# Kernel tuning notes

Measured on AMD Instinct MI355X. Metric: run time of the kernel, lower is better.

The kernel has to match this reference:

```python
import jax, jax.numpy as jnp
import numpy as np

B, S, H, E = 64, 1024, 256, 256

def setup_inputs() -> dict:
    key = jax.random.key(0)
    k = jax.random.split(key, 6)
    scale = 1.0 / np.sqrt(H)
    return {
        "data_alpha": jax.random.normal(k[0], (B, S, H), jnp.float32),
        "data_beta": jax.random.normal(k[1], (B, S, H), jnp.float32),
        "data_embed": jax.random.normal(k[2], (B, S, E), jnp.float32),
        "data_mask": jnp.ones((B, S), jnp.float32),
        "Wb": jax.random.normal(k[3], (E, H), jnp.float32) * scale,
        "bb": jnp.zeros((E,), jnp.float32),
        "Wa": jax.random.normal(k[4], (H,), jnp.float32) * scale,
        "ba": jnp.zeros((1,), jnp.float32),
    }

def reference(data_alpha, data_beta, data_embed, data_mask, Wb, bb, Wa, ba):
    # beta gates: tanh(Linear(H->E))  [B,S,E]
    beta_w = jnp.tanh(jnp.einsum('bsh,eh->bse', data_beta, Wb) + bb)
    # alpha logits: Linear(H->1)  [B,S]
    corr = jnp.einsum('bsh,h->bs', data_alpha, Wa) + ba
    attn = jnp.exp(corr)[:, None, :]                       # [B,1,S]
    seq = data_alpha.shape[1]
    flag = jnp.triu(jnp.ones((seq, seq), data_alpha.dtype))[None]  # j >= i
    ef = flag * data_mask[:, None, :]                      # [B,S,S]
    num = attn * ef                                        # [B,S,S]
    acc = jnp.sum(num, axis=-1, keepdims=True) + 1e-10     # [B,S,1]
    alpha = num / acc                                      # [B,S,S]
    ew = beta_w * data_embed                               # [B,S,E]
    return jnp.einsum('bij,bje->bie', alpha, ew)           # [B,S,E]
```

## Files before the change

kernel.cpp:

```cpp
#include <hip/hip_runtime.h>
#include <hip/hip_bf16.h>

#define B_ 64
#define S_ 1024
#define H_ 256
#define E_ 256

#define EG_ 32
#define LDSB_ST 264
#define CH_ 128
#define NCH_ 8

typedef __attribute__((ext_vector_type(8))) __bf16 bf16x8;
typedef __attribute__((ext_vector_type(4))) __bf16 bf16x4;
typedef __attribute__((ext_vector_type(4))) float f32x4;

__global__ __launch_bounds__(256) void k0_prep(
        const float* __restrict__ alpha, const float* __restrict__ mask,
        const float* __restrict__ Wa,    const float* __restrict__ ba,
        const float* __restrict__ Wb,    __bf16* __restrict__ WbBf,
        float* __restrict__ w) {
    const int tid = threadIdx.x, blk = blockIdx.x;
    if (blk < 64) {
        int i = blk * 256 + tid;
        float4 v = ((const float4*)Wb)[i];
        bf16x4 bv;
        bv[0] = (__bf16)v.x; bv[1] = (__bf16)v.y;
        bv[2] = (__bf16)v.z; bv[3] = (__bf16)v.w;
        ((bf16x4*)WbBf)[i] = bv;
    }
    const int pr = tid >> 2, pc = tid & 3;
    const int m = blk * 64 + pr;
    const float4* ar = (const float4*)(alpha + (size_t)m * H_ + pc * 64);
    const float4* wr = (const float4*)(Wa + pc * 64);
    float p = 0.f;
    #pragma unroll
    for (int i = 0; i < 16; ++i) {
        float4 a = ar[i], v = wr[i];
        p += a.x * v.x + a.y * v.y + a.z * v.z + a.w * v.w;
    }
    p += __shfl_xor(p, 1, 64);
    p += __shfl_xor(p, 2, 64);
    if (pc == 0) w[m] = __expf(p + ba[0]) * mask[m];
}

__global__ __launch_bounds__(512, 4) void k2_main(
        const float* __restrict__ beta, const float* __restrict__ embed,
        const __bf16* __restrict__ WbBf, const float* __restrict__ bb,
        const float* __restrict__ w, float* __restrict__ t) {
    __shared__ __bf16 ldsB[EG_ * LDSB_ST];
    __shared__ float wsLds[S_];
    __shared__ float ivLds[S_];
    __shared__ float red[8 * EG_];
    __shared__ float run[EG_];
    __shared__ float wsum[4];

    const int tid = threadIdx.x;
    const int wv = tid >> 6, lane = tid & 63;
    const int l15 = lane & 15, q = lane >> 4;
    const int blk = blockIdx.x;
    const int b  = (blk & 7) * 8 + (blk >> 6);
    const int eg = (blk >> 3) & 7;

    if (tid < 256)
        *(float4*)(wsLds + tid * 4) = *(const float4*)(w + b * S_ + tid * 4);
    {
        const int e = tid >> 4, ks = (tid & 15) * 16;
        const __bf16* src = WbBf + (size_t)(eg * EG_ + e) * H_ + ks;
        *(bf16x8*)(ldsB + e * LDSB_ST + ks)     = *(const bf16x8*)(src);
        *(bf16x8*)(ldsB + e * LDSB_ST + ks + 8) = *(const bf16x8*)(src + 8);
    }
    if (tid < EG_) run[tid] = 0.f;
    __syncthreads();

    {
        float w0 = 0, w1 = 0, w2 = 0, w3 = 0, tot = 0, suf = 0;
        const int sl = tid & 63, sw = tid >> 6;
        if (tid < 256) {
            w0 = wsLds[tid * 4];     w1 = wsLds[tid * 4 + 1];
            w2 = wsLds[tid * 4 + 2]; w3 = wsLds[tid * 4 + 3];
            tot = w0 + w1 + w2 + w3;
            suf = tot;
            #pragma unroll
            for (int off = 1; off < 64; off <<= 1) {
                float o = __shfl_down(suf, off, 64);
                if (sl + off < 64) suf += o;
            }
            if (sl == 0) wsum[sw] = suf;
        }
        __syncthreads();
        if (tid < 256) {
            float waveOff = 0.f;
            for (int j = sw + 1; j < 4; ++j) waveOff += wsum[j];
            float after = (suf - tot) + waveOff;
            float s3 = w3 + after, s2 = w2 + s3, s1 = w1 + s2, s0 = w0 + s1;
            ivLds[tid * 4]     = 1.f / (s0 + 1e-10f);
            ivLds[tid * 4 + 1] = 1.f / (s1 + 1e-10f);
            ivLds[tid * 4 + 2] = 1.f / (s2 + 1e-10f);
            ivLds[tid * 4 + 3] = 1.f / (s3 + 1e-10f);
        }
        __syncthreads();
    }

    const float bb0 = bb[eg * EG_ + l15];
    const float bb1 = bb[eg * EG_ + 16 + l15];

    for (int c = NCH_ - 1; c >= 0; --c) {
        const int rbase = c * CH_ + wv * 16;
        const float* Ar = beta + (size_t)(b * S_ + rbase + l15) * H_ + q * 8;

        f32x4 acc0 = {0.f, 0.f, 0.f, 0.f}, acc1 = {0.f, 0.f, 0.f, 0.f};
        #pragma unroll
        for (int kc = 0; kc < 8; ++kc) {
            float4 a0 = *(const float4*)(Ar + kc * 32);
            float4 a1 = *(const float4*)(Ar + kc * 32 + 4);
            bf16x8 af;
            af[0] = (__bf16)a0.x; af[1] = (__bf16)a0.y;
            af[2] = (__bf16)a0.z; af[3] = (__bf16)a0.w;
            af[4] = (__bf16)a1.x; af[5] = (__bf16)a1.y;
            af[6] = (__bf16)a1.z; af[7] = (__bf16)a1.w;
            bf16x8 bf0 = *(const bf16x8*)(ldsB + l15 * LDSB_ST + kc * 32 + q * 8);
            bf16x8 bf1 = *(const bf16x8*)(ldsB + (16 + l15) * LDSB_ST + kc * 32 + q * 8);
            acc0 = __builtin_amdgcn_mfma_f32_16x16x32_bf16(af, bf0, acc0, 0, 0, 0);
            acc1 = __builtin_amdgcn_mfma_f32_16x16x32_bf16(af, bf1, acc1, 0, 0, 0);
        }

        float sv0[4], sv1[4];
        {
            const int eG = eg * EG_ + l15;
            float tv[4];
            #pragma unroll
            for (int r = 0; r < 4; ++r) {
                const int m = c * CH_ + wv * 16 + q * 4 + r;
                float x = acc0[r] + bb0;
                x = fminf(fmaxf(x, -15.f), 15.f);
                float ex = __expf(2.f * x);
                float th = (ex - 1.f) / (ex + 1.f);
                tv[r] = wsLds[m] * th * embed[(size_t)(b * S_ + m) * E_ + eG];
            }
            float s3 = tv[3], s2 = tv[2] + s3, s1 = tv[1] + s2, s0 = tv[0] + s1;
            float g = s0;
            float g1 = __shfl_down(g, 16, 64);
            float g2 = __shfl_down(g, 32, 64);
            float g3 = __shfl_down(g, 48, 64);
            float addG = (q < 3 ? g1 : 0.f) + (q < 2 ? g2 : 0.f) + (q < 1 ? g3 : 0.f);
            if (q == 0) red[wv * EG_ + l15] = g + addG;
            sv0[0] = s0 + addG; sv0[1] = s1 + addG;
            sv0[2] = s2 + addG; sv0[3] = s3 + addG;
        }
        {
            const int eG = eg * EG_ + 16 + l15;
            float tv[4];
            #pragma unroll
            for (int r = 0; r < 4; ++r) {
                const int m = c * CH_ + wv * 16 + q * 4 + r;
                float x = acc1[r] + bb1;
                x = fminf(fmaxf(x, -15.f), 15.f);
                float ex = __expf(2.f * x);
                float th = (ex - 1.f) / (ex + 1.f);
                tv[r] = wsLds[m] * th * embed[(size_t)(b * S_ + m) * E_ + eG];
            }
            float s3 = tv[3], s2 = tv[2] + s3, s1 = tv[1] + s2, s0 = tv[0] + s1;
            float g = s0;
            float g1 = __shfl_down(g, 16, 64);
            float g2 = __shfl_down(g, 32, 64);
            float g3 = __shfl_down(g, 48, 64);
            float addG = (q < 3 ? g1 : 0.f) + (q < 2 ? g2 : 0.f) + (q < 1 ? g3 : 0.f);
            if (q == 0) red[wv * EG_ + 16 + l15] = g + addG;
            sv1[0] = s0 + addG; sv1[1] = s1 + addG;
            sv1[2] = s2 + addG; sv1[3] = s3 + addG;
        }
        __syncthreads();

        float nr0 = 0.f, nr1 = 0.f;
        {
            const int eG = eg * EG_ + l15;
            const float rn = run[l15];
            float later = rn, tot = 0.f;
            #pragma unroll
            for (int w2 = 0; w2 < 8; ++w2) {
                float v = red[w2 * EG_ + l15];
                tot += v;
                if (w2 > wv) later += v;
            }
            nr0 = rn + tot;
            #pragma unroll
            for (int r = 0; r < 4; ++r) {
                const int m = c * CH_ + wv * 16 + q * 4 + r;
                t[(size_t)(b * S_ + m) * E_ + eG] = (sv0[r] + later) * ivLds[m];
            }
        }
        {
            const int eG = eg * EG_ + 16 + l15;
            const float rn = run[16 + l15];
            float later = rn, tot = 0.f;
            #pragma unroll
            for (int w2 = 0; w2 < 8; ++w2) {
                float v = red[w2 * EG_ + 16 + l15];
                tot += v;
                if (w2 > wv) later += v;
            }
            nr1 = rn + tot;
            #pragma unroll
            for (int r = 0; r < 4; ++r) {
                const int m = c * CH_ + wv * 16 + q * 4 + r;
                t[(size_t)(b * S_ + m) * E_ + eG] = (sv1[r] + later) * ivLds[m];
            }
        }
        __syncthreads();
        if (wv == 0 && q == 0) {
            run[l15] = nr0;
            run[16 + l15] = nr1;
        }
    }
}

extern "C" void kernel_launch(void* const* d_in, const int* in_sizes, int n_in,
                              void* d_out, int out_size, void* d_ws, size_t ws_size,
                              hipStream_t stream) {
    const float* alpha = (const float*)d_in[0];
    const float* beta  = (const float*)d_in[1];
    const float* embed = (const float*)d_in[2];
    const float* mask  = (const float*)d_in[3];
    const float* Wb    = (const float*)d_in[4];
    const float* bbp   = (const float*)d_in[5];
    const float* Wa    = (const float*)d_in[6];
    const float* bap   = (const float*)d_in[7];

    float* t = (float*)d_out;

    char* ws = (char*)d_ws;
    float*  w    = (float*)ws;
    __bf16* WbBf = (__bf16*)(ws + (256 << 10));

    k0_prep<<<B_ * S_ / 64, 256, 0, stream>>>(alpha, mask, Wa, bap, Wb, WbBf, w);
    k2_main<<<B_ * (E_ / EG_), 512, 0, stream>>>(beta, embed, WbBf, bbp, w, t);
}
```

Measured before the change: 279.0 us.

## Fuse prep into main kernel, prefetch beta, double-buffer scan reduction

Merges the alpha-logit/Wb-conversion prep kernel into the main kernel, so each block computes exp weights for its batch directly into LDS and converts Wb to bf16 itself. Beta rows are software-prefetched one chunk ahead in registers, and embed loads are issued before the MFMA loop. The cross-wave reduction buffers are double-buffered, removing one block barrier per chunk. This removes a launch and the workspace round trip, but each of the 8 blocks per batch recomputes the alpha dot products, multiplying alpha reads.

New measurement: 287.1 us. 1.03x slower.

```diff
diff --git a/kernel.cpp b/kernel.cpp
--- a/kernel.cpp
+++ b/kernel.cpp
@@ -12,47 +12,19 @@
 #define NCH_ 8
 
 typedef __attribute__((ext_vector_type(8))) __bf16 bf16x8;
-typedef __attribute__((ext_vector_type(4))) __bf16 bf16x4;
 typedef __attribute__((ext_vector_type(4))) float f32x4;
 
-__global__ __launch_bounds__(256) void k0_prep(
-        const float* __restrict__ alpha, const float* __restrict__ mask,
+__global__ __launch_bounds__(512, 4) void k_all(
+        const float* __restrict__ alpha, const float* __restrict__ beta,
+        const float* __restrict__ embed, const float* __restrict__ mask,
+        const float* __restrict__ Wb,    const float* __restrict__ bb,
         const float* __restrict__ Wa,    const float* __restrict__ ba,
-        const float* __restrict__ Wb,    __bf16* __restrict__ WbBf,
-        float* __restrict__ w) {
-    const int tid = threadIdx.x, blk = blockIdx.x;
-    if (blk < 64) {
-        int i = blk * 256 + tid;
-        float4 v = ((const float4*)Wb)[i];
-        bf16x4 bv;
-        bv[0] = (__bf16)v.x; bv[1] = (__bf16)v.y;
-        bv[2] = (__bf16)v.z; bv[3] = (__bf16)v.w;
-        ((bf16x4*)WbBf)[i] = bv;
-    }
-    const int pr = tid >> 2, pc = tid & 3;
-    const int m = blk * 64 + pr;
-    const float4* ar = (const float4*)(alpha + (size_t)m * H_ + pc * 64);
-    const float4* wr = (const float4*)(Wa + pc * 64);
-    float p = 0.f;
-    #pragma unroll
-    for (int i = 0; i < 16; ++i) {
-        float4 a = ar[i], v = wr[i];
-        p += a.x * v.x + a.y * v.y + a.z * v.z + a.w * v.w;
-    }
-    p += __shfl_xor(p, 1, 64);
-    p += __shfl_xor(p, 2, 64);
-    if (pc == 0) w[m] = __expf(p + ba[0]) * mask[m];
-}
-
-__global__ __launch_bounds__(512, 4) void k2_main(
-        const float* __restrict__ beta, const float* __restrict__ embed,
-        const __bf16* __restrict__ WbBf, const float* __restrict__ bb,
-        const float* __restrict__ w, float* __restrict__ t) {
+        float* __restrict__ t) {
     __shared__ __bf16 ldsB[EG_ * LDSB_ST];
     __shared__ float wsLds[S_];
     __shared__ float ivLds[S_];
-    __shared__ float red[8 * EG_];
-    __shared__ float run[EG_];
+    __shared__ float red[2][8 * EG_];
+    __shared__ float run[2][EG_];
     __shared__ float wsum[4];
 
     const int tid = threadIdx.x;
@@ -62,15 +34,42 @@
     const int b  = (blk & 7) * 8 + (blk >> 6);
     const int eg = (blk >> 3) & 7;
 
-    if (tid < 256)
-        *(float4*)(wsLds + tid * 4) = *(const float4*)(w + b * S_ + tid * 4);
     {
-        const int e = tid >> 4, ks = (tid & 15) * 16;
-        const __bf16* src = WbBf + (size_t)(eg * EG_ + e) * H_ + ks;
-        *(bf16x8*)(ldsB + e * LDSB_ST + ks)     = *(const bf16x8*)(src);
-        *(bf16x8*)(ldsB + e * LDSB_ST + ks + 8) = *(const bf16x8*)(src + 8);
-    }
-    if (tid < EG_) run[tid] = 0.f;
+        const int e = tid >> 4, kq = (tid & 15) * 16;
+        const float4* src = (const float4*)(Wb + (size_t)(eg * EG_ + e) * H_ + kq);
+        float4 v0 = src[0], v1 = src[1], v2 = src[2], v3 = src[3];
+        bf16x8 p0, p1;
+        p0[0]=(__bf16)v0.x; p0[1]=(__bf16)v0.y; p0[2]=(__bf16)v0.z; p0[3]=(__bf16)v0.w;
+        p0[4]=(__bf16)v1.x; p0[5]=(__bf16)v1.y; p0[6]=(__bf16)v1.z; p0[7]=(__bf16)v1.w;
+        p1[0]=(__bf16)v2.x; p1[1]=(__bf16)v2.y; p1[2]=(__bf16)v2.z; p1[3]=(__bf16)v2.w;
+        p1[4]=(__bf16)v3.x; p1[5]=(__bf16)v3.y; p1[6]=(__bf16)v3.z; p1[7]=(__bf16)v3.w;
+        *(bf16x8*)(ldsB + e * LDSB_ST + kq)     = p0;
+        *(bf16x8*)(ldsB + e * LDSB_ST + kq + 8) = p1;
+    }
+
+    {
+        const int rsub = lane >> 4, pcl = lane & 15;
+        const float4* Wa4 = (const float4*)Wa;
+        float4 wa0 = Wa4[pcl], wa1 = Wa4[pcl + 16],
+               wa2 = Wa4[pcl + 32], wa3 = Wa4[pcl + 48];
+        const float ba0 = ba[0];
+        #pragma unroll 2
+        for (int ps = 0; ps < 32; ++ps) {
+            const int row = wv * 128 + ps * 4 + rsub;
+            const float4* ap = (const float4*)(alpha + ((size_t)b * S_ + row) * H_);
+            float4 x0 = ap[pcl], x1 = ap[pcl + 16], x2 = ap[pcl + 32], x3 = ap[pcl + 48];
+            float p = x0.x*wa0.x + x0.y*wa0.y + x0.z*wa0.z + x0.w*wa0.w
+                    + x1.x*wa1.x + x1.y*wa1.y + x1.z*wa1.z + x1.w*wa1.w
+                    + x2.x*wa2.x + x2.y*wa2.y + x2.z*wa2.z + x2.w*wa2.w
+                    + x3.x*wa3.x + x3.y*wa3.y + x3.z*wa3.z + x3.w*wa3.w;
+            p += __shfl_xor(p, 1, 64);
+            p += __shfl_xor(p, 2, 64);
+            p += __shfl_xor(p, 4, 64);
+            p += __shfl_xor(p, 8, 64);
+            if (pcl == 0) wsLds[row] = __expf(p + ba0) * mask[b * S_ + row];
+        }
+    }
+    if (tid < 64) run[tid >> 5][tid & 31] = 0.f;
     __syncthreads();
 
     {
@@ -104,16 +103,43 @@
 
     const float bb0 = bb[eg * EG_ + l15];
     const float bb1 = bb[eg * EG_ + 16 + l15];
-
+    const float* Arow0 = beta + ((size_t)b * S_ + wv * 16 + l15) * H_ + q * 8;
+    const size_t ebase = ((size_t)b * S_ + wv * 16 + q * 4) * E_ + eg * EG_;
+    const float* E0 = embed + ebase + l15;
+    const float* E1 = embed + ebase + 16 + l15;
+    float* T0 = t + ebase + l15;
+    float* T1 = t + ebase + 16 + l15;
+
+    float4 pa[4], pb[4];
+    #pragma unroll
+    for (int kc = 0; kc < 4; ++kc) {
+        pa[kc] = *(const float4*)(Arow0 + (size_t)(NCH_ - 1) * CH_ * H_ + kc * 32);
+        pb[kc] = *(const float4*)(Arow0 + (size_t)(NCH_ - 1) * CH_ * H_ + kc * 32 + 4);
+    }
+
+    int rb = 0;
     for (int c = NCH_ - 1; c >= 0; --c) {
-        const int rbase = c * CH_ + wv * 16;
-        const float* Ar = beta + (size_t)(b * S_ + rbase + l15) * H_ + q * 8;
+        const size_t coff = (size_t)c * CH_ * H_;
+        const size_t eoff = (size_t)c * CH_ * E_;
+
+        float e0[4], e1[4];
+        #pragma unroll
+        for (int r = 0; r < 4; ++r) {
+            e0[r] = E0[eoff + (size_t)r * E_];
+            e1[r] = E1[eoff + (size_t)r * E_];
+        }
+        float4 ha[4], hb[4];
+        #pragma unroll
+        for (int kc = 0; kc < 4; ++kc) {
+            ha[kc] = *(const float4*)(Arow0 + coff + (kc + 4) * 32);
+            hb[kc] = *(const float4*)(Arow0 + coff + (kc + 4) * 32 + 4);
+        }
 
         f32x4 acc0 = {0.f, 0.f, 0.f, 0.f}, acc1 = {0.f, 0.f, 0.f, 0.f};
         #pragma unroll
         for (int kc = 0; kc < 8; ++kc) {
-            float4 a0 = *(const float4*)(Ar + kc * 32);
-            float4 a1 = *(const float4*)(Ar + kc * 32 + 4);
+            float4 a0 = (kc < 4) ? pa[kc] : ha[kc - 4];
+            float4 a1 = (kc < 4) ? pb[kc] : hb[kc - 4];
             bf16x8 af;
             af[0] = (__bf16)a0.x; af[1] = (__bf16)a0.y;
             af[2] = (__bf16)a0.z; af[3] = (__bf16)a0.w;
@@ -125,18 +151,30 @@
             acc1 = __builtin_amdgcn_mfma_f32_16x16x32_bf16(af, bf1, acc1, 0, 0, 0);
         }
 
+        if (c > 0) {
+            #pragma unroll
+            for (int kc = 0; kc < 4; ++kc) {
+                pa[kc] = *(const float4*)(Arow0 + coff - (size_t)CH_ * H_ + kc * 32);
+                pb[kc] = *(const float4*)(Arow0 + coff - (size_t)CH_ * H_ + kc * 32 + 4);
+            }
+        }
+
+        float wmr[4], iv[4];
+        #pragma unroll
+        for (int r = 0; r < 4; ++r) {
+            wmr[r] = wsLds[c * CH_ + wv * 16 + q * 4 + r];
+            iv[r]  = ivLds[c * CH_ + wv * 16 + q * 4 + r];
+        }
         float sv0[4], sv1[4];
         {
-            const int eG = eg * EG_ + l15;
             float tv[4];
             #pragma unroll
             for (int r = 0; r < 4; ++r) {
-                const int m = c * CH_ + wv * 16 + q * 4 + r;
                 float x = acc0[r] + bb0;
                 x = fminf(fmaxf(x, -15.f), 15.f);
                 float ex = __expf(2.f * x);
                 float th = (ex - 1.f) / (ex + 1.f);
-                tv[r] = wsLds[m] * th * embed[(size_t)(b * S_ + m) * E_ + eG];
+                tv[r] = wmr[r] * th * e0[r];
             }
             float s3 = tv[3], s2 = tv[2] + s3, s1 = tv[1] + s2, s0 = tv[0] + s1;
             float g = s0;
@@ -144,21 +182,19 @@
             float g2 = __shfl_down(g, 32, 64);
             float g3 = __shfl_down(g, 48, 64);
             float addG = (q < 3 ? g1 : 0.f) + (q < 2 ? g2 : 0.f) + (q < 1 ? g3 : 0.f);
-            if (q == 0) red[wv * EG_ + l15] = g + addG;
+            if (q == 0) red[rb][wv * EG_ + l15] = g + addG;
             sv0[0] = s0 + addG; sv0[1] = s1 + addG;
             sv0[2] = s2 + addG; sv0[3] = s3 + addG;
         }
         {
-            const int eG = eg * EG_ + 16 + l15;
             float tv[4];
             #pragma unroll
             for (int r = 0; r < 4; ++r) {
-                const int m = c * CH_ + wv * 16 + q * 4 + r;
                 float x = acc1[r] + bb1;
                 x = fminf(fmaxf(x, -15.f), 15.f);
                 float ex = __expf(2.f * x);
                 float th = (ex - 1.f) / (ex + 1.f);
-                tv[r] = wsLds[m] * th * embed[(size_t)(b * S_ + m) * E_ + eG];
+                tv[r] = wmr[r] * th * e1[r];
             }
             float s3 = tv[3], s2 = tv[2] + s3, s1 = tv[1] + s2, s0 = tv[0] + s1;
             float g = s0;
@@ -166,52 +202,49 @@
             float g2 = __shfl_down(g, 32, 64);
             float g3 = __shfl_down(g, 48, 64);
             float addG = (q < 3 ? g1 : 0.f) + (q < 2 ? g2 : 0.f) + (q < 1 ? g3 : 0.f);
-            if (q == 0) red[wv * EG_ + 16 + l15] = g + addG;
+            if (q == 0) red[rb][wv * EG_ + 16 + l15] = g + addG;
             sv1[0] = s0 + addG; sv1[1] = s1 + addG;
             sv1[2] = s2 + addG; sv1[3] = s3 + addG;
         }
-        __syncthreads();
-
-        float nr0 = 0.f, nr1 = 0.f;
-        {
-            const int eG = eg * EG_ + l15;
-            const float rn = run[l15];
+
+        asm volatile("s_waitcnt lgkmcnt(0)" ::: "memory");
+        __builtin_amdgcn_s_barrier();
+        __builtin_amdgcn_sched_barrier(0);
+
+        float nr0, nr1;
+        {
+            const float rn = run[rb][l15];
             float later = rn, tot = 0.f;
             #pragma unroll
             for (int w2 = 0; w2 < 8; ++w2) {
-                float v = red[w2 * EG_ + l15];
+                float v = red[rb][w2 * EG_ + l15];
                 tot += v;
                 if (w2 > wv) later += v;
             }
             nr0 = rn + tot;
             #pragma unroll
-            for (int r = 0; r < 4; ++r) {
-                const int m = c * CH_ + wv * 16 + q * 4 + r;
-                t[(size_t)(b * S_ + m) * E_ + eG] = (sv0[r] + later) * ivLds[m];
-            }
-        }
-        {
-            const int eG = eg * EG_ + 16 + l15;
-            const float rn = run[16 + l15];
+            for (int r = 0; r < 4; ++r)
+                T0[eoff + (size_t)r * E_] = (sv0[r] + later) * iv[r];
+        }
+        {
+            const float rn = run[rb][16 + l15];
             float later = rn, tot = 0.f;
             #pragma unroll
             for (int w2 = 0; w2 < 8; ++w2) {
-                float v = red[w2 * EG_ + 16 + l15];
+                float v = red[rb][w2 * EG_ + 16 + l15];
                 tot += v;
                 if (w2 > wv) later += v;
             }
             nr1 = rn + tot;
             #pragma unroll
-            for (int r = 0; r < 4; ++r) {
-                const int m = c * CH_ + wv * 16 + q * 4 + r;
-                t[(size_t)(b * S_ + m) * E_ + eG] = (sv1[r] + later) * ivLds[m];
-            }
-        }
-        __syncthreads();
+            for (int r = 0; r < 4; ++r)
+                T1[eoff + (size_t)r * E_] = (sv1[r] + later) * iv[r];
+        }
         if (wv == 0 && q == 0) {
-            run[l15] = nr0;
-            run[16 + l15] = nr1;
-        }
+            run[rb ^ 1][l15] = nr0;
+            run[rb ^ 1][16 + l15] = nr1;
+        }
+        rb ^= 1;
     }
 }
 
@@ -227,12 +260,6 @@
     const float* Wa    = (const float*)d_in[6];
     const float* bap   = (const float*)d_in[7];
 
-    float* t = (float*)d_out;
-
-    char* ws = (char*)d_ws;
-    float*  w    = (float*)ws;
-    __bf16* WbBf = (__bf16*)(ws + (256 << 10));
-
-    k0_prep<<<B_ * S_ / 64, 256, 0, stream>>>(alpha, mask, Wa, bap, Wb, WbBf, w);
-    k2_main<<<B_ * (E_ / EG_), 512, 0, stream>>>(beta, embed, WbBf, bbp, w, t);
+    k_all<<<B_ * (E_ / EG_), 512, 0, stream>>>(alpha, beta, embed, mask,
+                                               Wb, bbp, Wa, bap, (float*)d_out);
 }
```

## Give each wave a contiguous row block and defer cross-wave scan to one sync

Applied to the files above, without the earlier changes.

The main kernel now assigns each wave a contiguous 128-row slab and walks it backwards, keeping the per-wave running suffix sums and partial results in registers. Only one barrier is needed to combine wave totals before all outputs are written, replacing the two barriers per chunk. Embed values are prefetched ahead of the MFMA loop. The prep kernel is also restructured so each wave reduces whole rows with 16 lanes and keeps Wa in registers, processing 128 rows per block. The trade-off is much higher register pressure (64 held partial sums per thread), which may reduce occupancy or cause spills.

Result: no change. 283.1 us (+1.5%).

```diff
diff --git a/kernel.cpp b/kernel.cpp
--- a/kernel.cpp
+++ b/kernel.cpp
@@ -8,8 +8,6 @@
 
 #define EG_ 32
 #define LDSB_ST 264
-#define CH_ 128
-#define NCH_ 8
 
 typedef __attribute__((ext_vector_type(8))) __bf16 bf16x8;
 typedef __attribute__((ext_vector_type(4))) __bf16 bf16x4;
@@ -29,19 +27,27 @@
         bv[2] = (__bf16)v.z; bv[3] = (__bf16)v.w;
         ((bf16x4*)WbBf)[i] = bv;
     }
-    const int pr = tid >> 2, pc = tid & 3;
-    const int m = blk * 64 + pr;
-    const float4* ar = (const float4*)(alpha + (size_t)m * H_ + pc * 64);
-    const float4* wr = (const float4*)(Wa + pc * 64);
-    float p = 0.f;
-    #pragma unroll
-    for (int i = 0; i < 16; ++i) {
-        float4 a = ar[i], v = wr[i];
-        p += a.x * v.x + a.y * v.y + a.z * v.z + a.w * v.w;
-    }
-    p += __shfl_xor(p, 1, 64);
-    p += __shfl_xor(p, 2, 64);
-    if (pc == 0) w[m] = __expf(p + ba[0]) * mask[m];
+    const int wv = tid >> 6, lane = tid & 63;
+    const int rsub = lane >> 4, pcl = lane & 15;
+    const float4* Wa4 = (const float4*)Wa;
+    float4 wa0 = Wa4[pcl], wa1 = Wa4[pcl + 16],
+           wa2 = Wa4[pcl + 32], wa3 = Wa4[pcl + 48];
+    const float ba0 = ba[0];
+    #pragma unroll 2
+    for (int ps = 0; ps < 8; ++ps) {
+        const int m = blk * 128 + ps * 16 + wv * 4 + rsub;
+        const float4* ap = (const float4*)(alpha + (size_t)m * H_);
+        float4 x0 = ap[pcl], x1 = ap[pcl + 16], x2 = ap[pcl + 32], x3 = ap[pcl + 48];
+        float p = x0.x*wa0.x + x0.y*wa0.y + x0.z*wa0.z + x0.w*wa0.w
+                + x1.x*wa1.x + x1.y*wa1.y + x1.z*wa1.z + x1.w*wa1.w
+                + x2.x*wa2.x + x2.y*wa2.y + x2.z*wa2.z + x2.w*wa2.w
+                + x3.x*wa3.x + x3.y*wa3.y + x3.z*wa3.z + x3.w*wa3.w;
+        p += __shfl_xor(p, 1, 64);
+        p += __shfl_xor(p, 2, 64);
+        p += __shfl_xor(p, 4, 64);
+        p += __shfl_xor(p, 8, 64);
+        if (pcl == 0) w[m] = __expf(p + ba0) * mask[m];
+    }
 }
 
 __global__ __launch_bounds__(512, 4) void k2_main(
@@ -51,8 +57,7 @@
     __shared__ __bf16 ldsB[EG_ * LDSB_ST];
     __shared__ float wsLds[S_];
     __shared__ float ivLds[S_];
-    __shared__ float red[8 * EG_];
-    __shared__ float run[EG_];
+    __shared__ float red[8][EG_];
     __shared__ float wsum[4];
 
     const int tid = threadIdx.x;
@@ -62,15 +67,14 @@
     const int b  = (blk & 7) * 8 + (blk >> 6);
     const int eg = (blk >> 3) & 7;
 
+    {
+        const int e = tid >> 4, kq = (tid & 15) * 16;
+        const __bf16* src = WbBf + (size_t)(eg * EG_ + e) * H_ + kq;
+        *(bf16x8*)(ldsB + e * LDSB_ST + kq)     = *(const bf16x8*)(src);
+        *(bf16x8*)(ldsB + e * LDSB_ST + kq + 8) = *(const bf16x8*)(src + 8);
+    }
     if (tid < 256)
         *(float4*)(wsLds + tid * 4) = *(const float4*)(w + b * S_ + tid * 4);
-    {
-        const int e = tid >> 4, ks = (tid & 15) * 16;
-        const __bf16* src = WbBf + (size_t)(eg * EG_ + e) * H_ + ks;
-        *(bf16x8*)(ldsB + e * LDSB_ST + ks)     = *(const bf16x8*)(src);
-        *(bf16x8*)(ldsB + e * LDSB_ST + ks + 8) = *(const bf16x8*)(src + 8);
-    }
-    if (tid < EG_) run[tid] = 0.f;
     __syncthreads();
 
     {
@@ -104,16 +108,34 @@
 
     const float bb0 = bb[eg * EG_ + l15];
     const float bb1 = bb[eg * EG_ + 16 + l15];
-
-    for (int c = NCH_ - 1; c >= 0; --c) {
-        const int rbase = c * CH_ + wv * 16;
-        const float* Ar = beta + (size_t)(b * S_ + rbase + l15) * H_ + q * 8;
+    const float* Arow = beta + ((size_t)b * S_ + wv * 128 + l15) * H_ + q * 8;
+    const size_t ebase = ((size_t)b * S_ + wv * 128 + q * 4) * E_ + eg * EG_;
+    const float* E0 = embed + ebase + l15;
+    const float* E1 = E0 + 16;
+    float* T0 = t + ebase + l15;
+    float* T1 = T0 + 16;
+
+    float sv0[8][4], sv1[8][4];
+    float run0 = 0.f, run1 = 0.f;
+
+    #pragma unroll
+    for (int si = 0; si < 8; ++si) {
+        const int st = 7 - si;
+        const size_t aoff = (size_t)st * 16 * H_;
+        const size_t eoff = (size_t)st * 16 * E_;
+
+        float e0[4], e1[4];
+        #pragma unroll
+        for (int r = 0; r < 4; ++r) {
+            e0[r] = E0[eoff + (size_t)r * E_];
+            e1[r] = E1[eoff + (size_t)r * E_];
+        }
 
         f32x4 acc0 = {0.f, 0.f, 0.f, 0.f}, acc1 = {0.f, 0.f, 0.f, 0.f};
         #pragma unroll
         for (int kc = 0; kc < 8; ++kc) {
-            float4 a0 = *(const float4*)(Ar + kc * 32);
-            float4 a1 = *(const float4*)(Ar + kc * 32 + 4);
+            float4 a0 = *(const float4*)(Arow + aoff + kc * 32);
+            float4 a1 = *(const float4*)(Arow + aoff + kc * 32 + 4);
             bf16x8 af;
             af[0] = (__bf16)a0.x; af[1] = (__bf16)a0.y;
             af[2] = (__bf16)a0.z; af[3] = (__bf16)a0.w;
@@ -125,18 +147,19 @@
             acc1 = __builtin_amdgcn_mfma_f32_16x16x32_bf16(af, bf1, acc1, 0, 0, 0);
         }
 
-        float sv0[4], sv1[4];
+        float wmr[4];
+        #pragma unroll
+        for (int r = 0; r < 4; ++r)
+            wmr[r] = wsLds[wv * 128 + st * 16 + q * 4 + r];
         {
-            const int eG = eg * EG_ + l15;
             float tv[4];
             #pragma unroll
             for (int r = 0; r < 4; ++r) {
-                const int m = c * CH_ + wv * 16 + q * 4 + r;
                 float x = acc0[r] + bb0;
                 x = fminf(fmaxf(x, -15.f), 15.f);
                 float ex = __expf(2.f * x);
                 float th = (ex - 1.f) / (ex + 1.f);
-                tv[r] = wsLds[m] * th * embed[(size_t)(b * S_ + m) * E_ + eG];
+                tv[r] = wmr[r] * th * e0[r];
             }
             float s3 = tv[3], s2 = tv[2] + s3, s1 = tv[1] + s2, s0 = tv[0] + s1;
             float g = s0;
@@ -144,21 +167,23 @@
             float g2 = __shfl_down(g, 32, 64);
             float g3 = __shfl_down(g, 48, 64);
             float addG = (q < 3 ? g1 : 0.f) + (q < 2 ? g2 : 0.f) + (q < 1 ? g3 : 0.f);
-            if (q == 0) red[wv * EG_ + l15] = g + addG;
-            sv0[0] = s0 + addG; sv0[1] = s1 + addG;
-            sv0[2] = s2 + addG; sv0[3] = s3 + addG;
+            float top = s0 + addG;
+            float tot = __shfl(top, l15, 64);
+            sv0[si][0] = s0 + addG + run0;
+            sv0[si][1] = s1 + addG + run0;
+            sv0[si][2] = s2 + addG + run0;
+            sv0[si][3] = s3 + addG + run0;
+            run0 += tot;
         }
         {
-            const int eG = eg * EG_ + 16 + l15;
             float tv[4];
             #pragma unroll
             for (int r = 0; r < 4; ++r) {
-                const int m = c * CH_ + wv * 16 + q * 4 + r;
                 float x = acc1[r] + bb1;
                 x = fminf(fmaxf(x, -15.f), 15.f);
                 float ex = __expf(2.f * x);
                 float th = (ex - 1.f) / (ex + 1.f);
-                tv[r] = wsLds[m] * th * embed[(size_t)(b * S_ + m) * E_ + eG];
+                tv[r] = wmr[r] * th * e1[r];
             }
             float s3 = tv[3], s2 = tv[2] + s3, s1 = tv[1] + s2, s0 = tv[0] + s1;
             float g = s0;
@@ -166,51 +191,42 @@
             float g2 = __shfl_down(g, 32, 64);
             float g3 = __shfl_down(g, 48, 64);
             float addG = (q < 3 ? g1 : 0.f) + (q < 2 ? g2 : 0.f) + (q < 1 ? g3 : 0.f);
-            if (q == 0) red[wv * EG_ + 16 + l15] = g + addG;
-            sv1[0] = s0 + addG; sv1[1] = s1 + addG;
-            sv1[2] = s2 + addG; sv1[3] = s3 + addG;
-        }
-        __syncthreads();
-
-        float nr0 = 0.f, nr1 = 0.f;
-        {
-            const int eG = eg * EG_ + l15;
-            const float rn = run[l15];
-            float later = rn, tot = 0.f;
-            #pragma unroll
-            for (int w2 = 0; w2 < 8; ++w2) {
-                float v = red[w2 * EG_ + l15];
-                tot += v;
-                if (w2 > wv) later += v;
-            }
-            nr0 = rn + tot;
-            #pragma unroll
-            for (int r = 0; r < 4; ++r) {
-                const int m = c * CH_ + wv * 16 + q * 4 + r;
-                t[(size_t)(b * S_ + m) * E_ + eG] = (sv0[r] + later) * ivLds[m];
-            }
-        }
-        {
-            const int eG = eg * EG_ + 16 + l15;
-            const float rn = run[16 + l15];
-            float later = rn, tot = 0.f;
-            #pragma unroll
-            for (int w2 = 0; w2 < 8; ++w2) {
-                float v = red[w2 * EG_ + 16 + l15];
-                tot += v;
-                if (w2 > wv) later += v;
-            }
-            nr1 = rn + tot;
-            #pragma unroll
-            for (int r = 0; r < 4; ++r) {
-                const int m = c * CH_ + wv * 16 + q * 4 + r;
-                t[(size_t)(b * S_ + m) * E_ + eG] = (sv1[r] + later) * ivLds[m];
-            }
-        }
-        __syncthreads();
-        if (wv == 0 && q == 0) {
-            run[l15] = nr0;
-            run[16 + l15] = nr1;
+            float top = s0 + addG;
+            float tot = __shfl(top, l15, 64);
+            sv1[si][0] = s0 + addG + run1;
+            sv1[si][1] = s1 + addG + run1;
+            sv1[si][2] = s2 + addG + run1;
+            sv1[si][3] = s3 + addG + run1;
+            run1 += tot;
+        }
+    }
+
+    if (q == 0) {
+        red[wv][l15] = run0;
+        red[wv][16 + l15] = run1;
+    }
+    __syncthreads();
+    float c0 = 0.f, c1 = 0.f;
+    #pragma unroll
+    for (int w2 = 0; w2 < 8; ++w2) {
+        if (w2 > wv) {
+            c0 += red[w2][l15];
+            c1 += red[w2][16 + l15];
+        }
+    }
+
+    #pragma unroll
+    for (int si = 0; si < 8; ++si) {
+        const int st = 7 - si;
+        const size_t eoff = (size_t)st * 16 * E_;
+        float iv[4];
+        #pragma unroll
+        for (int r = 0; r < 4; ++r)
+            iv[r] = ivLds[wv * 128 + st * 16 + q * 4 + r];
+        #pragma unroll
+        for (int r = 0; r < 4; ++r) {
+            T0[eoff + (size_t)r * E_] = (sv0[si][r] + c0) * iv[r];
+            T1[eoff + (size_t)r * E_] = (sv1[si][r] + c1) * iv[r];
         }
     }
 }
@@ -227,12 +243,11 @@
     const float* Wa    = (const float*)d_in[6];
     const float* bap   = (const float*)d_in[7];
 
-    float* t = (float*)d_out;
-
     char* ws = (char*)d_ws;
     float*  w    = (float*)ws;
     __bf16* WbBf = (__bf16*)(ws + (256 << 10));
 
-    k0_prep<<<B_ * S_ / 64, 256, 0, stream>>>(alpha, mask, Wa, bap, Wb, WbBf, w);
-    k2_main<<<B_ * (E_ / EG_), 512, 0, stream>>>(beta, embed, WbBf, bbp, w, t);
+    k0_prep<<<B_ * S_ / 128, 256, 0, stream>>>(alpha, mask, Wa, bap, Wb, WbBf, w);
+    k2_main<<<B_ * (E_ / EG_), 512, 0, stream>>>(beta, embed, WbBf, bbp, w,
+                                                 (float*)d_out);
 }
```

## Pre-convert beta to bf16 in prep kernel and prefetch chunks in main kernel

Applied to the files above, without the earlier changes.

The prep kernel now also converts the whole beta tensor to bf16 in workspace, so the main kernel, which rereads beta once per embedding group, streams half the bytes. The main kernel prefetches the next chunk's A fragments into registers, loads embed early, and double-buffers the reduction arrays to drop one barrier per chunk. This adds an extra pass writing and reading a 32MB bf16 copy, and falls back to the old path if the workspace is too small.

Result: faster. 264.7 us (-5.1%).

```diff
diff --git a/kernel.cpp b/kernel.cpp
--- a/kernel.cpp
+++ b/kernel.cpp
@@ -18,33 +18,247 @@
 __global__ __launch_bounds__(256) void k0_prep(
         const float* __restrict__ alpha, const float* __restrict__ mask,
         const float* __restrict__ Wa,    const float* __restrict__ ba,
-        const float* __restrict__ Wb,    __bf16* __restrict__ WbBf,
+        const float* __restrict__ Wb,    const float* __restrict__ beta,
+        __bf16* __restrict__ WbBf,       __bf16* __restrict__ betaBf,
         float* __restrict__ w) {
     const int tid = threadIdx.x, blk = blockIdx.x;
+    if (blk >= 512) {
+        const int base = (blk - 512) * 256 + tid;
+        #pragma unroll 4
+        for (int i = 0; i < 32; ++i) {
+            const int idx = base + i * 131072;
+            float4 v = ((const float4*)beta)[idx];
+            bf16x4 bv;
+            bv[0]=(__bf16)v.x; bv[1]=(__bf16)v.y; bv[2]=(__bf16)v.z; bv[3]=(__bf16)v.w;
+            ((bf16x4*)betaBf)[idx] = bv;
+        }
+        return;
+    }
     if (blk < 64) {
         int i = blk * 256 + tid;
         float4 v = ((const float4*)Wb)[i];
         bf16x4 bv;
-        bv[0] = (__bf16)v.x; bv[1] = (__bf16)v.y;
-        bv[2] = (__bf16)v.z; bv[3] = (__bf16)v.w;
+        bv[0]=(__bf16)v.x; bv[1]=(__bf16)v.y; bv[2]=(__bf16)v.z; bv[3]=(__bf16)v.w;
         ((bf16x4*)WbBf)[i] = bv;
     }
-    const int pr = tid >> 2, pc = tid & 3;
-    const int m = blk * 64 + pr;
-    const float4* ar = (const float4*)(alpha + (size_t)m * H_ + pc * 64);
-    const float4* wr = (const float4*)(Wa + pc * 64);
-    float p = 0.f;
+    const int wv = tid >> 6, lane = tid & 63;
+    const int rsub = lane >> 4, pcl = lane & 15;
+    const float4* Wa4 = (const float4*)Wa;
+    float4 wa0 = Wa4[pcl], wa1 = Wa4[pcl + 16],
+           wa2 = Wa4[pcl + 32], wa3 = Wa4[pcl + 48];
+    const float ba0 = ba[0];
+    #pragma unroll 2
+    for (int ps = 0; ps < 8; ++ps) {
+        const int m = blk * 128 + ps * 16 + wv * 4 + rsub;
+        const float4* ap = (const float4*)(alpha + (size_t)m * H_);
+        float4 x0 = ap[pcl], x1 = ap[pcl + 16], x2 = ap[pcl + 32], x3 = ap[pcl + 48];
+        float p = x0.x*wa0.x + x0.y*wa0.y + x0.z*wa0.z + x0.w*wa0.w
+                + x1.x*wa1.x + x1.y*wa1.y + x1.z*wa1.z + x1.w*wa1.w
+                + x2.x*wa2.x + x2.y*wa2.y + x2.z*wa2.z + x2.w*wa2.w
+                + x3.x*wa3.x + x3.y*wa3.y + x3.z*wa3.z + x3.w*wa3.w;
+        p += __shfl_xor(p, 1, 64);
+        p += __shfl_xor(p, 2, 64);
+        p += __shfl_xor(p, 4, 64);
+        p += __shfl_xor(p, 8, 64);
+        if (pcl == 0) w[m] = __expf(p + ba0) * mask[m];
+    }
+}
+
+__global__ __launch_bounds__(512, 4) void k2_bf(
+        const __bf16* __restrict__ betaBf, const float* __restrict__ embed,
+        const __bf16* __restrict__ WbBf,   const float* __restrict__ bb,
+        const float* __restrict__ w,       float* __restrict__ t) {
+    __shared__ __bf16 ldsB[EG_ * LDSB_ST];
+    __shared__ float wsLds[S_];
+    __shared__ float ivLds[S_];
+    __shared__ float red[2][8 * EG_];
+    __shared__ float run[2][EG_];
+    __shared__ float wsum[4];
+
+    const int tid = threadIdx.x;
+    const int wv = tid >> 6, lane = tid & 63;
+    const int l15 = lane & 15, q = lane >> 4;
+    const int blk = blockIdx.x;
+    const int b  = (blk & 7) * 8 + (blk >> 6);
+    const int eg = (blk >> 3) & 7;
+
+    {
+        const int e = tid >> 4, kq = (tid & 15) * 16;
+        const __bf16* src = WbBf + (size_t)(eg * EG_ + e) * H_ + kq;
+        *(bf16x8*)(ldsB + e * LDSB_ST + kq)     = *(const bf16x8*)(src);
+        *(bf16x8*)(ldsB + e * LDSB_ST + kq + 8) = *(const bf16x8*)(src + 8);
+    }
+    if (tid < 256)
+        *(float4*)(wsLds + tid * 4) = *(const float4*)(w + b * S_ + tid * 4);
+    if (tid < 64) run[tid >> 5][tid & 31] = 0.f;
+    __syncthreads();
+
+    {
+        float w0 = 0, w1 = 0, w2 = 0, w3 = 0, tot = 0, suf = 0;
+        const int sl = tid & 63, sw = tid >> 6;
+        if (tid < 256) {
+            w0 = wsLds[tid * 4];     w1 = wsLds[tid * 4 + 1];
+            w2 = wsLds[tid * 4 + 2]; w3 = wsLds[tid * 4 + 3];
+            tot = w0 + w1 + w2 + w3;
+            suf = tot;
+            #pragma unroll
+            for (int off = 1; off < 64; off <<= 1) {
+                float o = __shfl_down(suf, off, 64);
+                if (sl + off < 64) suf += o;
+            }
+            if (sl == 0) wsum[sw] = suf;
+        }
+        __syncthreads();
+        if (tid < 256) {
+            float waveOff = 0.f;
+            for (int j = sw + 1; j < 4; ++j) waveOff += wsum[j];
+            float after = (suf - tot) + waveOff;
+            float s3 = w3 + after, s2 = w2 + s3, s1 = w1 + s2, s0 = w0 + s1;
+            ivLds[tid * 4]     = 1.f / (s0 + 1e-10f);
+            ivLds[tid * 4 + 1] = 1.f / (s1 + 1e-10f);
+            ivLds[tid * 4 + 2] = 1.f / (s2 + 1e-10f);
+            ivLds[tid * 4 + 3] = 1.f / (s3 + 1e-10f);
+        }
+        __syncthreads();
+    }
+
+    const float bb0 = bb[eg * EG_ + l15];
+    const float bb1 = bb[eg * EG_ + 16 + l15];
+    const __bf16* Abase = betaBf + ((size_t)b * S_ + wv * 16 + l15) * H_ + q * 8;
+    const size_t ebase = ((size_t)b * S_ + wv * 16 + q * 4) * E_ + eg * EG_;
+    const float* E0 = embed + ebase + l15;
+    const float* E1 = E0 + 16;
+    float* T0 = t + ebase + l15;
+    float* T1 = T0 + 16;
+
+    bf16x8 nA[8];
+    {
+        const size_t coff = (size_t)(NCH_ - 1) * CH_ * H_;
+        #pragma unroll
+        for (int kc = 0; kc < 8; ++kc)
+            nA[kc] = *(const bf16x8*)(Abase + coff + (size_t)kc * 32);
+    }
+
     #pragma unroll
-    for (int i = 0; i < 16; ++i) {
-        float4 a = ar[i], v = wr[i];
-        p += a.x * v.x + a.y * v.y + a.z * v.z + a.w * v.w;
-    }
-    p += __shfl_xor(p, 1, 64);
-    p += __shfl_xor(p, 2, 64);
-    if (pc == 0) w[m] = __expf(p + ba[0]) * mask[m];
+    for (int si = 0; si < 8; ++si) {
+        const int c = 7 - si;
+        const int rb = si & 1;
+        const size_t eoff = (size_t)c * CH_ * E_;
+
+        bf16x8 curA[8];
+        #pragma unroll
+        for (int kc = 0; kc < 8; ++kc) curA[kc] = nA[kc];
+
+        float e0[4], e1[4];
+        #pragma unroll
+        for (int r = 0; r < 4; ++r) {
+            e0[r] = E0[eoff + (size_t)r * E_];
+            e1[r] = E1[eoff + (size_t)r * E_];
+        }
+
+        if (c > 0) {
+            const size_t poff = (size_t)(c - 1) * CH_ * H_;
+            #pragma unroll
+            for (int kc = 0; kc < 8; ++kc)
+                nA[kc] = *(const bf16x8*)(Abase + poff + (size_t)kc * 32);
+        }
+
+        f32x4 acc0 = {0.f, 0.f, 0.f, 0.f}, acc1 = {0.f, 0.f, 0.f, 0.f};
+        #pragma unroll
+        for (int kc = 0; kc < 8; ++kc) {
+            bf16x8 bf0 = *(const bf16x8*)(ldsB + l15 * LDSB_ST + kc * 32 + q * 8);
+            bf16x8 bf1 = *(const bf16x8*)(ldsB + (16 + l15) * LDSB_ST + kc * 32 + q * 8);
+            acc0 = __builtin_amdgcn_mfma_f32_16x16x32_bf16(curA[kc], bf0, acc0, 0, 0, 0);
+            acc1 = __builtin_amdgcn_mfma_f32_16x16x32_bf16(curA[kc], bf1, acc1, 0, 0, 0);
+        }
+
+        float wmr[4], iv[4];
+        #pragma unroll
+        for (int r = 0; r < 4; ++r) {
+            wmr[r] = wsLds[c * CH_ + wv * 16 + q * 4 + r];
+            iv[r]  = ivLds[c * CH_ + wv * 16 + q * 4 + r];
+        }
+        float sv0[4], sv1[4];
+        {
+            float tv[4];
+            #pragma unroll
+            for (int r = 0; r < 4; ++r) {
+                float x = acc0[r] + bb0;
+                x = fminf(fmaxf(x, -15.f), 15.f);
+                float ex = __expf(2.f * x);
+                tv[r] = wmr[r] * ((ex - 1.f) / (ex + 1.f)) * e0[r];
+            }
+            float s3 = tv[3], s2 = tv[2] + s3, s1 = tv[1] + s2, s0 = tv[0] + s1;
+            float g = s0;
+            float g1 = __shfl_down(g, 16, 64);
+            float g2 = __shfl_down(g, 32, 64);
+            float g3 = __shfl_down(g, 48, 64);
+            float addG = (q < 3 ? g1 : 0.f) + (q < 2 ? g2 : 0.f) + (q < 1 ? g3 : 0.f);
+            if (q == 0) red[rb][wv * EG_ + l15] = g + addG;
+            sv0[0] = s0 + addG; sv0[1] = s1 + addG;
+            sv0[2] = s2 + addG; sv0[3] = s3 + addG;
+        }
+        {
+            float tv[4];
+            #pragma unroll
+            for (int r = 0; r < 4; ++r) {
+                float x = acc1[r] + bb1;
+                x = fminf(fmaxf(x, -15.f), 15.f);
+                float ex = __expf(2.f * x);
+                tv[r] = wmr[r] * ((ex - 1.f) / (ex + 1.f)) * e1[r];
+            }
+            float s3 = tv[3], s2 = tv[2] + s3, s1 = tv[1] + s2, s0 = tv[0] + s1;
+            float g = s0;
+            float g1 = __shfl_down(g, 16, 64);
+            float g2 = __shfl_down(g, 32, 64);
+            float g3 = __shfl_down(g, 48, 64);
+            float addG = (q < 3 ? g1 : 0.f) + (q < 2 ? g2 : 0.f) + (q < 1 ? g3 : 0.f);
+            if (q == 0) red[rb][wv * EG_ + 16 + l15] = g + addG;
+            sv1[0] = s0 + addG; sv1[1] = s1 + addG;
+            sv1[2] = s2 + addG; sv1[3] = s3 + addG;
+        }
+
+        asm volatile("s_waitcnt lgkmcnt(0)" ::: "memory");
+        __builtin_amdgcn_s_barrier();
+        __builtin_amdgcn_sched_barrier(0);
+
+        float nr0, nr1;
+        {
+            const float rn = run[rb][l15];
+            float later = rn, tot = 0.f;
+            #pragma unroll
+            for (int w2 = 0; w2 < 8; ++w2) {
+                float v = red[rb][w2 * EG_ + l15];
+                tot += v;
+                if (w2 > wv) later += v;
+            }
+            nr0 = rn + tot;
+            #pragma unroll
+            for (int r = 0; r < 4; ++r)
+                T0[eoff + (size_t)r * E_] = (sv0[r] + later) * iv[r];
+        }
+        {
+            const float rn = run[rb][16 + l15];
+            float later = rn, tot = 0.f;
+            #pragma unroll
+            for (int w2 = 0; w2 < 8; ++w2) {
+                float v = red[rb][w2 * EG_ + 16 + l15];
+                tot += v;
+                if (w2 > wv) later += v;
+            }
+            nr1 = rn + tot;
+            #pragma unroll
+            for (int r = 0; r < 4; ++r)
+                T1[eoff + (size_t)r * E_] = (sv1[r] + later) * iv[r];
+        }
+        if (wv == 0 && q == 0) {
+            run[rb ^ 1][l15] = nr0;
+            run[rb ^ 1][16 + l15] = nr1;
+        }
+    }
 }
 
-__global__ __launch_bounds__(512, 4) void k2_main(
+__global__ __launch_bounds__(512, 4) void k2_f32(
         const float* __restrict__ beta, const float* __restrict__ embed,
         const __bf16* __restrict__ WbBf, const float* __restrict__ bb,
         const float* __restrict__ w, float* __restrict__ t) {
@@ -72,7 +286,6 @@
     }
     if (tid < EG_) run[tid] = 0.f;
     __syncthreads();
-
     {
         float w0 = 0, w1 = 0, w2 = 0, w3 = 0, tot = 0, suf = 0;
         const int sl = tid & 63, sw = tid >> 6;
@@ -101,14 +314,11 @@
         }
         __syncthreads();
     }
-
     const float bb0 = bb[eg * EG_ + l15];
     const float bb1 = bb[eg * EG_ + 16 + l15];
-
     for (int c = NCH_ - 1; c >= 0; --c) {
         const int rbase = c * CH_ + wv * 16;
         const float* Ar = beta + (size_t)(b * S_ + rbase + l15) * H_ + q * 8;
-
         f32x4 acc0 = {0.f, 0.f, 0.f, 0.f}, acc1 = {0.f, 0.f, 0.f, 0.f};
         #pragma unroll
         for (int kc = 0; kc < 8; ++kc) {
@@ -124,10 +334,8 @@
             acc0 = __builtin_amdgcn_mfma_f32_16x16x32_bf16(af, bf0, acc0, 0, 0, 0);
             acc1 = __builtin_amdgcn_mfma_f32_16x16x32_bf16(af, bf1, acc1, 0, 0, 0);
         }
-
         float sv0[4], sv1[4];
         {
-            const int eG = eg * EG_ + l15;
             float tv[4];
             #pragma unroll
             for (int r = 0; r < 4; ++r) {
@@ -135,8 +343,8 @@
                 float x = acc0[r] + bb0;
                 x = fminf(fmaxf(x, -15.f), 15.f);
                 float ex = __expf(2.f * x);
-                float th = (ex - 1.f) / (ex + 1.f);
-                tv[r] = wsLds[m] * th * embed[(size_t)(b * S_ + m) * E_ + eG];
+                tv[r] = wsLds[m] * ((ex - 1.f) / (ex + 1.f))
+                        * embed[(size_t)(b * S_ + m) * E_ + eg * EG_ + l15];
             }
             float s3 = tv[3], s2 = tv[2] + s3, s1 = tv[1] + s2, s0 = tv[0] + s1;
             float g = s0;
@@ -149,7 +357,6 @@
             sv0[2] = s2 + addG; sv0[3] = s3 + addG;
         }
         {
-            const int eG = eg * EG_ + 16 + l15;
             float tv[4];
             #pragma unroll
             for (int r = 0; r < 4; ++r) {
@@ -157,8 +364,8 @@
                 float x = acc1[r] + bb1;
                 x = fminf(fmaxf(x, -15.f), 15.f);
                 float ex = __expf(2.f * x);
-                float th = (ex - 1.f) / (ex + 1.f);
-                tv[r] = wsLds[m] * th * embed[(size_t)(b * S_ + m) * E_ + eG];
+                tv[r] = wsLds[m] * ((ex - 1.f) / (ex + 1.f))
+                        * embed[(size_t)(b * S_ + m) * E_ + eg * EG_ + 16 + l15];
             }
             float s3 = tv[3], s2 = tv[2] + s3, s1 = tv[1] + s2, s0 = tv[0] + s1;
             float g = s0;
@@ -171,10 +378,8 @@
             sv1[2] = s2 + addG; sv1[3] = s3 + addG;
         }
         __syncthreads();
-
-        float nr0 = 0.f, nr1 = 0.f;
-        {
-            const int eG = eg * EG_ + l15;
+        float nr0, nr1;
+        {
             const float rn = run[l15];
             float later = rn, tot = 0.f;
             #pragma unroll
@@ -187,11 +392,11 @@
             #pragma unroll
             for (int r = 0; r < 4; ++r) {
                 const int m = c * CH_ + wv * 16 + q * 4 + r;
-                t[(size_t)(b * S_ + m) * E_ + eG] = (sv0[r] + later) * ivLds[m];
-            }
-        }
-        {
-            const int eG = eg * EG_ + 16 + l15;
+                t[(size_t)(b * S_ + m) * E_ + eg * EG_ + l15]
+                    = (sv0[r] + later) * ivLds[m];
+            }
+        }
+        {
             const float rn = run[16 + l15];
             float later = rn, tot = 0.f;
             #pragma unroll
@@ -204,7 +409,8 @@
             #pragma unroll
             for (int r = 0; r < 4; ++r) {
                 const int m = c * CH_ + wv * 16 + q * 4 + r;
-                t[(size_t)(b * S_ + m) * E_ + eG] = (sv1[r] + later) * ivLds[m];
+                t[(size_t)(b * S_ + m) * E_ + eg * EG_ + 16 + l15]
+                    = (sv1[r] + later) * ivLds[m];
             }
         }
         __syncthreads();
@@ -227,12 +433,21 @@
     const float* Wa    = (const float*)d_in[6];
     const float* bap   = (const float*)d_in[7];
 
-    float* t = (float*)d_out;
-
     char* ws = (char*)d_ws;
-    float*  w    = (float*)ws;
-    __bf16* WbBf = (__bf16*)(ws + (256 << 10));
-
-    k0_prep<<<B_ * S_ / 64, 256, 0, stream>>>(alpha, mask, Wa, bap, Wb, WbBf, w);
-    k2_main<<<B_ * (E_ / EG_), 512, 0, stream>>>(beta, embed, WbBf, bbp, w, t);
+    float*  w      = (float*)ws;
+    __bf16* WbBf   = (__bf16*)(ws + (256 << 10));
+    __bf16* betaBf = (__bf16*)(ws + (512 << 10));
+    const size_t need = (512 << 10) + (size_t)B_ * S_ * H_ * sizeof(__bf16);
+
+    if (ws_size >= need) {
+        k0_prep<<<1024, 256, 0, stream>>>(alpha, mask, Wa, bap, Wb, beta,
+                                          WbBf, betaBf, w);
+        k2_bf<<<B_ * (E_ / EG_), 512, 0, stream>>>(betaBf, embed, WbBf, bbp, w,
+                                                   (float*)d_out);
+    } else {
+        k0_prep<<<512, 256, 0, stream>>>(alpha, mask, Wa, bap, Wb, beta,
+                                         WbBf, betaBf, w);
+        k2_f32<<<B_ * (E_ / EG_), 512, 0, stream>>>(beta, embed, WbBf, bbp, w,
+                                                    (float*)d_out);
+    }
 }
```
